# Optimization experiments

Measured on AMD Instinct MI355X. Metric: run time of the kernel, lower is better.

## Reference

```python
import jax, jax.numpy as jnp
import numpy as np

B, C, H, W = 16, 512, 32, 32
KC = C // 8  # key_channels = 64


def setup_inputs() -> dict:
    key = jax.random.key(0)
    ks = jax.random.split(key, 6)
    s_in = 1.0 / np.sqrt(C)
    return {
        "x": jax.random.normal(ks[0], (B, C, H, W), dtype=jnp.float32),
        "Wq": jax.random.normal(ks[1], (KC, C), dtype=jnp.float32) * s_in,
        "bq": jnp.zeros((KC,), dtype=jnp.float32),
        "Wk": jax.random.normal(ks[2], (KC, C), dtype=jnp.float32) * s_in,
        "bk": jnp.zeros((KC,), dtype=jnp.float32),
        "Wv": jax.random.normal(ks[3], (C, C), dtype=jnp.float32) * s_in,
        "bv": jnp.zeros((C,), dtype=jnp.float32),
        "Wo": jax.random.normal(ks[4], (C, C), dtype=jnp.float32) * s_in,
        "bo": jnp.zeros((C,), dtype=jnp.float32),
        "gamma": jnp.zeros((1,), dtype=jnp.float32),
    }


def reference(x, Wq, bq, Wk, bk, Wv, bv, Wo, bo, gamma):
    b, c, h, w = x.shape
    n = h * w
    kc = Wq.shape[0]
    xf = x.reshape(b, c, n)  # [B, C, N]
    # 1x1 convs == channel matmuls
    q = jnp.einsum('kc,bcn->bnk', Wq, xf) + bq  # [B, N, KC]
    k = jnp.einsum('kc,bcn->bkn', Wk, xf) + bk[None, :, None]  # [B, KC, N]
    v = jnp.einsum('vc,bcn->bnv', Wv, xf) + bv  # [B, N, C]
    scale = jnp.asarray(kc, x.dtype) ** -0.5
    att = jax.nn.softmax(jnp.einsum('bnk,bkm->bnm', q, k) * scale, axis=-1)  # [B, N, N]
    out = jnp.einsum('bnm,bmv->bnv', att, v)  # [B, N, C]
    out = jnp.einsum('cv,bnv->bcn', Wo, out) + bo[None, :, None]  # [B, C, N]
    out = gamma[0] * out + xf
    return out.reshape(b, c, h, w)
```

## Files before the change

### kernel.cpp

```cpp
#include <hip/hip_runtime.h>
#include <cstddef>


typedef unsigned short ushort_t;
typedef __attribute__((ext_vector_type(8))) short bf16x8;
typedef __attribute__((ext_vector_type(4))) float f32x4;

#define QSCALE 0.18033688011112042f

__device__ __forceinline__ ushort_t f2bf_t(float f) {
  return (ushort_t)(__float_as_uint(f) >> 16);
}
__device__ __forceinline__ unsigned pk2bf(float lo, float hi) {
  return __builtin_amdgcn_perm(__float_as_uint(hi), __float_as_uint(lo),
                               0x07060302u);
}

__device__ __forceinline__ void gload16(const ushort_t* g, ushort_t* l) {
  __builtin_amdgcn_global_load_lds(
      (const __attribute__((address_space(1))) void*)g,
      (__attribute__((address_space(3))) void*)l, 16, 0, 0);
}

template <int TM>
__device__ __forceinline__ void gemm_core(
    const ushort_t* __restrict__ A, int lda,
    const ushort_t* __restrict__ B, int ldb,
    int K, int m0, int n0,
    ushort_t* As, ushort_t* Bs, f32x4 (*acc)[4])
{
  constexpr int MT  = TM / 32;
  constexpr int WTM = TM / 2;
  const int t = threadIdx.x;
  const int lane = t & 63, quad = lane >> 4, l15 = lane & 15;
  const int w = t >> 6, wm = w >> 1, wn = w & 1;
  const int rr = (lane >> 3) & 7;
  const int gg = (lane & 7) ^ rr;

  #pragma unroll
  for (int i = 0; i < MT; ++i)
    #pragma unroll
    for (int j = 0; j < 4; ++j) acc[i][j] = (f32x4){0.f, 0.f, 0.f, 0.f};

  for (int k0 = 0; k0 < K; k0 += 64) {
    #pragma unroll
    for (int i = 0; i < TM / 32; ++i) {
      const int mrow = w * (TM / 4) + i * 8;
      gload16(A + (size_t)(m0 + mrow + rr) * lda + k0 + gg * 8, As + mrow * 64);
    }
    #pragma unroll
    for (int i = 0; i < 4; ++i) {
      const int mrow = w * 32 + i * 8;
      gload16(B + (size_t)(n0 + mrow + rr) * ldb + k0 + gg * 8, Bs + mrow * 64);
    }
    __syncthreads();
    #pragma unroll
    for (int kk = 0; kk < 2; ++kk) {
      const int gq = kk * 4 + quad;
      const int sg = (gq ^ (l15 & 7)) * 8;
      bf16x8 af[MT], bfr[4];
      #pragma unroll
      for (int i = 0; i < MT; ++i)
        af[i] = *(const bf16x8*)(As + (wm * WTM + i * 16 + l15) * 64 + sg);
      #pragma unroll
      for (int j = 0; j < 4; ++j)
        bfr[j] = *(const bf16x8*)(Bs + (wn * 64 + j * 16 + l15) * 64 + sg);
      #pragma unroll
      for (int i = 0; i < MT; ++i)
        #pragma unroll
        for (int j = 0; j < 4; ++j)
          acc[i][j] = __builtin_amdgcn_mfma_f32_16x16x32_bf16(
              af[i], bfr[j], acc[i][j], 0, 0, 0);
    }
    __syncthreads();
  }
}

template <int TM, class F>
__device__ __forceinline__ void store_bf16(
    ushort_t* lds, ushort_t* __restrict__ out, int ldo, int m0, int n0,
    f32x4 (*acc)[4], F f)
{
  constexpr int MT = TM / 32, WTM = TM / 2, SI = TM / 16;
  const int t = threadIdx.x;
  const int lane = t & 63, quad = lane >> 4, l15 = lane & 15;
  const int w = t >> 6, wm = w >> 1, wn = w & 1;
  #pragma unroll
  for (int i = 0; i < MT; ++i)
    #pragma unroll
    for (int j = 0; j < 4; ++j)
      #pragma unroll
      for (int r = 0; r < 4; ++r) {
        const int rl = wm * WTM + i * 16 + quad * 4 + r;
        const int cl = wn * 64 + j * 16 + l15;
        lds[rl * 136 + cl] = f2bf_t(f(i, j, r, rl, cl, acc[i][j][r]));
      }
  __syncthreads();
  #pragma unroll
  for (int i = 0; i < SI; ++i) {
    const int s = i * 256 + t, m = s >> 4, g = s & 15;
    const uint4 v = *(const uint4*)(lds + m * 136 + g * 8);
    *(uint4*)(out + (size_t)(m0 + m) * ldo + n0 + g * 8) = v;
  }
}

__global__ __launch_bounds__(256) void prep_x(
    const float* __restrict__ x,
    const float* __restrict__ Wq, const float* __restrict__ Wk,
    const float* __restrict__ Wv, const float* __restrict__ Wo,
    ushort_t* __restrict__ xbfT, ushort_t* __restrict__ Wqk,
    ushort_t* __restrict__ Wvb, ushort_t* __restrict__ Wob)
{
  __shared__ float T[64][65];
  const int t = threadIdx.x;
  if (blockIdx.y == 8) {
    const int id = blockIdx.z * 16 + blockIdx.x;
    #pragma unroll
    for (int p = 0; p < 5; ++p) {
      const int s = p * 256 + t;
      if (s < 1152) {
        const int u = id * 1152 + s;
        const int e = u * 2;
        float f0, f1;
        if (e < 32768)       { f0 = Wq[e];         f1 = Wq[e + 1]; }
        else if (e < 65536)  { f0 = Wk[e - 32768]; f1 = Wk[e - 32767]; }
        else if (e < 327680) { f0 = Wv[e - 65536]; f1 = Wv[e - 65535]; }
        else                 { f0 = Wo[e - 327680]; f1 = Wo[e - 327679]; }
        const unsigned pk = pk2bf(f0, f1);
        if (e < 65536)       *((unsigned*)Wqk + u) = pk;
        else if (e < 327680) *((unsigned*)Wvb + (u - 32768)) = pk;
        else                 *((unsigned*)Wob + (u - 163840)) = pk;
      }
    }
    return;
  }
  const int b = blockIdx.z, c0 = blockIdx.y * 64, n0 = blockIdx.x * 64;
  const float* xb = x + ((size_t)b * 512 + c0) * 1024 + n0;
  const int nj = t & 63, ci0 = t >> 6;
  #pragma unroll
  for (int p = 0; p < 16; ++p) {
    const int ci = p * 4 + ci0;
    T[ci][nj] = xb[(size_t)ci * 1024 + nj];
  }
  __syncthreads();
  const int c2 = (t & 31) * 2, nr0 = t >> 5;
  #pragma unroll
  for (int p = 0; p < 8; ++p) {
    const int nr = p * 8 + nr0;
    *(unsigned*)&xbfT[((size_t)b * 1024 + n0 + nr) * 512 + c0 + c2] =
        pk2bf(T[c2][nr], T[c2 + 1][nr]);
  }
}

__global__ __launch_bounds__(256) void k1_fused(
    const ushort_t* __restrict__ xbfT, const ushort_t* __restrict__ Wqk,
    const ushort_t* __restrict__ Wvb,
    const float* __restrict__ bq, const float* __restrict__ bk,
    const float* __restrict__ bv,
    ushort_t* __restrict__ qkt, ushort_t* __restrict__ vt2)
{
  __shared__ __align__(16) ushort_t lds[17408];
  const int bid = blockIdx.x;
  const int t = threadIdx.x, lane = t & 63, quad = lane >> 4, l15 = lane & 15;
  const int w = t >> 6, wm = w >> 1, wn = w & 1;
  if (bid < 512) {
    const int b = bid >> 5, my = (bid >> 3) & 3, nx = bid & 7;
    const int m0 = my * 128, n0 = nx * 128;
    f32x4 acc[4][4];
    gemm_core<128>(Wvb, 512, xbfT + (size_t)b * 524288, 512, 512, m0, n0,
                   lds, lds + 128 * 64, acc);
    float br[4][4];
    #pragma unroll
    for (int i = 0; i < 4; ++i)
      #pragma unroll
      for (int r = 0; r < 4; ++r)
        br[i][r] = bv[m0 + wm * 64 + i * 16 + quad * 4 + r];
    store_bf16<128>(lds, vt2 + (size_t)b * 524288, 1024, m0, n0, acc,
        [&](int i, int, int r, int, int, float v) { return v + br[i][r]; });
  } else {
    const int id = bid - 512, b = id >> 4, my = id & 15;
    const int m0 = my * 64;
    f32x4 acc[2][4];
    gemm_core<64>(xbfT + (size_t)b * 524288, 512, Wqk, 512, 512, m0, 0,
                  lds, lds + 64 * 64, acc);
    float bc[4], qs[4];
    #pragma unroll
    for (int j = 0; j < 4; ++j) {
      const int col = wn * 64 + j * 16 + l15;
      bc[j] = (col < 64) ? bq[col] : bk[col - 64];
      qs[j] = (col < 64) ? QSCALE : 1.0f;
    }
    store_bf16<64>(lds, qkt + (size_t)b * 131072, 128, m0, 0, acc,
        [&](int, int j, int, int, int, float v) { return (v + bc[j]) * qs[j]; });
  }
}

__global__ __launch_bounds__(256) void flash_attn(
    const ushort_t* __restrict__ qkt, const ushort_t* __restrict__ vt2,
    ushort_t* __restrict__ o1)
{
  __shared__ __align__(16) ushort_t buf[16896];
  __shared__ float lsum[64][2];
  ushort_t* Ks = buf;
  ushort_t* Vs = buf + 4096;
  ushort_t* Ps = buf + 12288;

  const int t = threadIdx.x;
  const int lane = t & 63, quad = lane >> 4, l15 = lane & 15;
  const int w = t >> 6, wm = w >> 1, wn = w & 1;
  const int rr = (lane >> 3) & 7, gg = (lane & 7) ^ rr;

  const unsigned lin = blockIdx.x;
  const unsigned wid = (lin & 7) * 128 + (lin >> 3);
  const int b  = wid >> 6;
  const int m0 = ((wid >> 2) & 15) * 64;
  const int c0 = (wid & 3) * 128;

  const ushort_t* qb = qkt + (size_t)b * 131072;
  const ushort_t* vb = vt2 + (size_t)b * 524288;

  #pragma unroll
  for (int i = 0; i < 2; ++i) {
    const int mrow = w * 16 + i * 8;
    gload16(qb + (size_t)(m0 + mrow + rr) * 128 + gg * 8, Ps + mrow * 64);
  }
  __syncthreads();
  bf16x8 af_q[2][2];
  #pragma unroll
  for (int kk = 0; kk < 2; ++kk) {
    const int sg = ((kk * 4 + quad) ^ (l15 & 7)) * 8;
    #pragma unroll
    for (int i = 0; i < 2; ++i)
      af_q[i][kk] = *(const bf16x8*)(Ps + (wm * 32 + i * 16 + l15) * 64 + sg);
  }

  f32x4 accO[2][4];
  #pragma unroll
  for (int i = 0; i < 2; ++i)
    #pragma unroll
    for (int j = 0; j < 4; ++j) accO[i][j] = (f32x4){0.f, 0.f, 0.f, 0.f};
  float rsum[2][4] = {{0.f, 0.f, 0.f, 0.f}, {0.f, 0.f, 0.f, 0.f}};

  ushort_t* ps_w = Ps + (wm * 32 + quad * 4) * 72 + wn * 32 + l15;

  #pragma unroll 1
  for (int mc = 0; mc < 1024; mc += 64) {
    __syncthreads();
    #pragma unroll
    for (int i = 0; i < 2; ++i) {
      const int mrow = w * 16 + i * 8;
      gload16(qb + (size_t)(mc + mrow + rr) * 128 + 64 + gg * 8, Ks + mrow * 64);
    }
    #pragma unroll
    for (int i = 0; i < 4; ++i) {
      const int mrow = w * 32 + i * 8;
      gload16(vb + (size_t)(c0 + mrow + rr) * 1024 + mc + gg * 8, Vs + mrow * 64);
    }
    __syncthreads();

    f32x4 accS[2][2];
    #pragma unroll
    for (int i = 0; i < 2; ++i)
      #pragma unroll
      for (int j = 0; j < 2; ++j) accS[i][j] = (f32x4){0.f, 0.f, 0.f, 0.f};
    #pragma unroll
    for (int kk = 0; kk < 2; ++kk) {
      const int sg = ((kk * 4 + quad) ^ (l15 & 7)) * 8;
      bf16x8 bk_[2];
      #pragma unroll
      for (int j = 0; j < 2; ++j)
        bk_[j] = *(const bf16x8*)(Ks + (wn * 32 + j * 16 + l15) * 64 + sg);
      #pragma unroll
      for (int i = 0; i < 2; ++i)
        #pragma unroll
        for (int j = 0; j < 2; ++j)
          accS[i][j] = __builtin_amdgcn_mfma_f32_16x16x32_bf16(
              af_q[i][kk], bk_[j], accS[i][j], 0, 0, 0);
    }
    #pragma unroll
    for (int i = 0; i < 2; ++i)
      #pragma unroll
      for (int j = 0; j < 2; ++j)
        #pragma unroll
        for (int r = 0; r < 4; ++r) {
          const float e = exp2f(accS[i][j][r]);
          rsum[i][r] += e;
          ps_w[(i * 16 + r) * 72 + j * 16] = f2bf_t(e);
        }
    __syncthreads();

    #pragma unroll
    for (int kk = 0; kk < 2; ++kk) {
      const int gq = kk * 4 + quad;
      const int sgv = (gq ^ (l15 & 7)) * 8;
      bf16x8 ap[2], bv_[4];
      #pragma unroll
      for (int i = 0; i < 2; ++i)
        ap[i] = *(const bf16x8*)(Ps + (wm * 32 + i * 16 + l15) * 72 + gq * 8);
      #pragma unroll
      for (int j = 0; j < 4; ++j)
        bv_[j] = *(const bf16x8*)(Vs + (wn * 64 + j * 16 + l15) * 64 + sgv);
      #pragma unroll
      for (int i = 0; i < 2; ++i)
        #pragma unroll
        for (int j = 0; j < 4; ++j)
          accO[i][j] = __builtin_amdgcn_mfma_f32_16x16x32_bf16(
              ap[i], bv_[j], accO[i][j], 0, 0, 0);
    }
  }

  #pragma unroll
  for (int i = 0; i < 2; ++i)
    #pragma unroll
    for (int r = 0; r < 4; ++r) {
      float s = rsum[i][r];
      #pragma unroll
      for (int d = 1; d < 16; d <<= 1) s += __shfl_xor(s, d, 16);
      if (l15 == 0) lsum[wm * 32 + i * 16 + quad * 4 + r][wn] = s;
    }
  __syncthreads();

  ushort_t* fl_b = buf;
  #pragma unroll
  for (int i = 0; i < 2; ++i)
    #pragma unroll
    for (int r = 0; r < 4; ++r) {
      const int row = wm * 32 + i * 16 + quad * 4 + r;
      const float inv = 1.0f / (lsum[row][0] + lsum[row][1]);
      #pragma unroll
      for (int j = 0; j < 4; ++j)
        fl_b[row * 136 + wn * 64 + j * 16 + l15] = f2bf_t(accO[i][j][r] * inv);
    }
  __syncthreads();
  #pragma unroll
  for (int p = 0; p < 4; ++p) {
    const int s = p * 256 + t, m = s >> 4, g = s & 15;
    const uint4 v = *(const uint4*)(fl_b + m * 136 + g * 8);
    *(uint4*)(o1 + ((size_t)b * 1024 + m0 + m) * 512 + c0 + g * 8) = v;
  }
}

__global__ __launch_bounds__(256) void k4_proj(
    const ushort_t* __restrict__ Wob, const ushort_t* __restrict__ o1,
    const float* __restrict__ bo, const float* __restrict__ gamma,
    const float* __restrict__ x, float* __restrict__ out)
{
  __shared__ __align__(16) ushort_t lds[128 * 136];
  const int b = blockIdx.z, m0 = blockIdx.y * 128, n0 = blockIdx.x * 128;
  f32x4 acc[4][4];
  gemm_core<128>(Wob, 512, o1 + (size_t)b * 524288, 512, 512, m0, n0,
                 lds, lds + 128 * 64, acc);
  const int t = threadIdx.x, lane = t & 63, quad = lane >> 4, l15 = lane & 15;
  const int w = t >> 6, wm = w >> 1, wn = w & 1;
  const float g = gamma[0];
  float br[4][4];
  #pragma unroll
  for (int i = 0; i < 4; ++i)
    #pragma unroll
    for (int r = 0; r < 4; ++r)
      br[i][r] = bo[m0 + wm * 64 + i * 16 + quad * 4 + r];
  float* fl = (float*)lds;
  #pragma unroll
  for (int h = 0; h < 2; ++h) {
    if (wm == h) {
      #pragma unroll
      for (int i = 0; i < 4; ++i)
        #pragma unroll
        for (int j = 0; j < 4; ++j)
          #pragma unroll
          for (int r = 0; r < 4; ++r)
            fl[(i * 16 + quad * 4 + r) * 132 + wn * 64 + j * 16 + l15] =
                g * (acc[i][j][r] + br[i][r]);
    }
    __syncthreads();
    #pragma unroll
    for (int i2 = 0; i2 < 8; ++i2) {
      const int s = i2 * 256 + t, m = s >> 5, c4 = s & 31;
      f32x4 v = *(const f32x4*)(fl + m * 132 + c4 * 4);
      const size_t gi = ((size_t)b * 512 + m0 + h * 64 + m) * 1024 + n0 + c4 * 4;
      const f32x4 xr = *(const f32x4*)(x + gi);
      v += xr;
      *(f32x4*)(out + gi) = v;
    }
    __syncthreads();
  }
}

extern "C" void kernel_launch(void* const* d_in, const int* in_sizes, int n_in,
                              void* d_out, int out_size, void* d_ws, size_t ws_size,
                              hipStream_t stream) {
  const float* x     = (const float*)d_in[0];
  const float* Wq    = (const float*)d_in[1];
  const float* bq    = (const float*)d_in[2];
  const float* Wk    = (const float*)d_in[3];
  const float* bk    = (const float*)d_in[4];
  const float* Wv    = (const float*)d_in[5];
  const float* bv    = (const float*)d_in[6];
  const float* Wo    = (const float*)d_in[7];
  const float* bo    = (const float*)d_in[8];
  const float* gamma = (const float*)d_in[9];
  float* out = (float*)d_out;

  char* wsp = (char*)d_ws;
  ushort_t* xbfT   = (ushort_t*)wsp;  wsp += (size_t)16 * 1024 * 512 * 2;
  ushort_t* Wqk_bf = (ushort_t*)wsp;  wsp += (size_t)128 * 512 * 2;
  ushort_t* Wv_bf  = (ushort_t*)wsp;  wsp += (size_t)512 * 512 * 2;
  ushort_t* Wo_bf  = (ushort_t*)wsp;  wsp += (size_t)512 * 512 * 2;
  ushort_t* qkt    = (ushort_t*)wsp;  wsp += (size_t)16 * 1024 * 128 * 2;
  ushort_t* vt2    = (ushort_t*)wsp;  wsp += (size_t)16 * 512 * 1024 * 2;
  ushort_t* o1     = xbfT;

  prep_x    <<<dim3(16, 9, 16), 256, 0, stream>>>(x, Wq, Wk, Wv, Wo,
                                                  xbfT, Wqk_bf, Wv_bf, Wo_bf);
  k1_fused  <<<768, 256, 0, stream>>>(xbfT, Wqk_bf, Wv_bf, bq, bk, bv, qkt, vt2);
  flash_attn<<<dim3(1024), 256, 0, stream>>>(qkt, vt2, o1);
  k4_proj   <<<dim3(8, 4, 16), 256, 0, stream>>>(Wo_bf, o1, bo, gamma, x, out);
}
```

Before: 195.6 us.

## Double-buffer K/V tiles in flash attention to overlap loads with compute

The flash attention loop now keeps two LDS buffers for the K, V and P tiles and issues the next tile's global-to-LDS loads before computing on the current one. The old per-iteration load-then-sync pattern is replaced by explicit waitcnt plus barrier pairs, cutting one barrier per iteration. It also swaps exp2f for the raw hardware exp2 builtin. LDS use roughly doubles, which may lower occupancy, and the manual waitcnt placement must stay correct.

```diff
diff --git a/kernel.cpp b/kernel.cpp
--- a/kernel.cpp
+++ b/kernel.cpp
@@ -199,11 +199,11 @@
     const ushort_t* __restrict__ qkt, const ushort_t* __restrict__ vt2,
     ushort_t* __restrict__ o1)
 {
-  __shared__ __align__(16) ushort_t buf[16896];
+  __shared__ __align__(16) ushort_t buf[33792];
   __shared__ float lsum[64][2];
-  ushort_t* Ks = buf;
-  ushort_t* Vs = buf + 4096;
-  ushort_t* Ps = buf + 12288;
+  ushort_t* Ks0 = buf;
+  ushort_t* Vs0 = buf + 8192;
+  ushort_t* Ps0 = buf + 24576;
 
   const int t = threadIdx.x;
   const int lane = t & 63, quad = lane >> 4, l15 = lane & 15;
@@ -222,17 +222,31 @@
   #pragma unroll
   for (int i = 0; i < 2; ++i) {
     const int mrow = w * 16 + i * 8;
-    gload16(qb + (size_t)(m0 + mrow + rr) * 128 + gg * 8, Ps + mrow * 64);
-  }
-  __syncthreads();
+    gload16(qb + (size_t)(m0 + mrow + rr) * 128 + gg * 8, Ps0 + mrow * 64);
+  }
+  asm volatile("s_waitcnt vmcnt(0)" ::: "memory");
+  __builtin_amdgcn_s_barrier();
+
   bf16x8 af_q[2][2];
   #pragma unroll
   for (int kk = 0; kk < 2; ++kk) {
     const int sg = ((kk * 4 + quad) ^ (l15 & 7)) * 8;
     #pragma unroll
     for (int i = 0; i < 2; ++i)
-      af_q[i][kk] = *(const bf16x8*)(Ps + (wm * 32 + i * 16 + l15) * 64 + sg);
-  }
+      af_q[i][kk] = *(const bf16x8*)(Ps0 + (wm * 32 + i * 16 + l15) * 64 + sg);
+  }
+
+  const ushort_t* kp = qb + (size_t)(w * 16 + rr) * 128 + 64 + gg * 8;
+  const ushort_t* vp = vb + (size_t)(c0 + w * 32 + rr) * 1024 + gg * 8;
+
+  #pragma unroll
+  for (int i = 0; i < 2; ++i)
+    gload16(kp + i * 1024, Ks0 + (w * 16 + i * 8) * 64);
+  #pragma unroll
+  for (int i = 0; i < 4; ++i)
+    gload16(vp + i * 8192, Vs0 + (w * 32 + i * 8) * 64);
+  asm volatile("s_waitcnt vmcnt(0) lgkmcnt(0)" ::: "memory");
+  __builtin_amdgcn_s_barrier();
 
   f32x4 accO[2][4];
   #pragma unroll
@@ -241,22 +255,30 @@
     for (int j = 0; j < 4; ++j) accO[i][j] = (f32x4){0.f, 0.f, 0.f, 0.f};
   float rsum[2][4] = {{0.f, 0.f, 0.f, 0.f}, {0.f, 0.f, 0.f, 0.f}};
 
-  ushort_t* ps_w = Ps + (wm * 32 + quad * 4) * 72 + wn * 32 + l15;
+  const int psw_off = (wm * 32 + quad * 4) * 72 + wn * 32 + l15;
+  const int sg0 = (quad ^ (l15 & 7)) * 8;
+  const int sg1 = ((4 + quad) ^ (l15 & 7)) * 8;
+
+  const ushort_t* kpn = kp + 8192;
+  const ushort_t* vpn = vp + 64;
+  int p = 0;
 
   #pragma unroll 1
   for (int mc = 0; mc < 1024; mc += 64) {
-    __syncthreads();
-    #pragma unroll
-    for (int i = 0; i < 2; ++i) {
-      const int mrow = w * 16 + i * 8;
-      gload16(qb + (size_t)(mc + mrow + rr) * 128 + 64 + gg * 8, Ks + mrow * 64);
-    }
-    #pragma unroll
-    for (int i = 0; i < 4; ++i) {
-      const int mrow = w * 32 + i * 8;
-      gload16(vb + (size_t)(c0 + mrow + rr) * 1024 + mc + gg * 8, Vs + mrow * 64);
-    }
-    __syncthreads();
+    ushort_t* Ksd = p ? Ks0 + 4096 : Ks0;
+    ushort_t* Vsd = p ? Vs0 + 8192 : Vs0;
+    ushort_t* Psd = p ? Ps0 + 4608 : Ps0;
+    ushort_t* Ksn = p ? Ks0 : Ks0 + 4096;
+    ushort_t* Vsn = p ? Vs0 : Vs0 + 8192;
+
+    if (mc < 960) {
+      #pragma unroll
+      for (int i = 0; i < 2; ++i)
+        gload16(kpn + i * 1024, Ksn + (w * 16 + i * 8) * 64);
+      #pragma unroll
+      for (int i = 0; i < 4; ++i)
+        gload16(vpn + i * 8192, Vsn + (w * 32 + i * 8) * 64);
+    }
 
     f32x4 accS[2][2];
     #pragma unroll
@@ -265,11 +287,11 @@
       for (int j = 0; j < 2; ++j) accS[i][j] = (f32x4){0.f, 0.f, 0.f, 0.f};
     #pragma unroll
     for (int kk = 0; kk < 2; ++kk) {
-      const int sg = ((kk * 4 + quad) ^ (l15 & 7)) * 8;
+      const int sg = kk ? sg1 : sg0;
       bf16x8 bk_[2];
       #pragma unroll
       for (int j = 0; j < 2; ++j)
-        bk_[j] = *(const bf16x8*)(Ks + (wn * 32 + j * 16 + l15) * 64 + sg);
+        bk_[j] = *(const bf16x8*)(Ksd + (wn * 32 + j * 16 + l15) * 64 + sg);
       #pragma unroll
       for (int i = 0; i < 2; ++i)
         #pragma unroll
@@ -277,29 +299,33 @@
           accS[i][j] = __builtin_amdgcn_mfma_f32_16x16x32_bf16(
               af_q[i][kk], bk_[j], accS[i][j], 0, 0, 0);
     }
+
+    ushort_t* psw = Psd + psw_off;
     #pragma unroll
     for (int i = 0; i < 2; ++i)
       #pragma unroll
       for (int j = 0; j < 2; ++j)
         #pragma unroll
         for (int r = 0; r < 4; ++r) {
-          const float e = exp2f(accS[i][j][r]);
+          const float e = __builtin_amdgcn_exp2f(accS[i][j][r]);
           rsum[i][r] += e;
-          ps_w[(i * 16 + r) * 72 + j * 16] = f2bf_t(e);
+          psw[(i * 16 + r) * 72 + j * 16] = f2bf_t(e);
         }
-    __syncthreads();
+
+    asm volatile("s_waitcnt lgkmcnt(0)" ::: "memory");
+    __builtin_amdgcn_s_barrier();
 
     #pragma unroll
     for (int kk = 0; kk < 2; ++kk) {
       const int gq = kk * 4 + quad;
-      const int sgv = (gq ^ (l15 & 7)) * 8;
+      const int sgv = kk ? sg1 : sg0;
       bf16x8 ap[2], bv_[4];
       #pragma unroll
       for (int i = 0; i < 2; ++i)
-        ap[i] = *(const bf16x8*)(Ps + (wm * 32 + i * 16 + l15) * 72 + gq * 8);
+        ap[i] = *(const bf16x8*)(Psd + (wm * 32 + i * 16 + l15) * 72 + gq * 8);
       #pragma unroll
       for (int j = 0; j < 4; ++j)
-        bv_[j] = *(const bf16x8*)(Vs + (wn * 64 + j * 16 + l15) * 64 + sgv);
+        bv_[j] = *(const bf16x8*)(Vsd + (wn * 64 + j * 16 + l15) * 64 + sgv);
       #pragma unroll
       for (int i = 0; i < 2; ++i)
         #pragma unroll
@@ -307,6 +333,13 @@
           accO[i][j] = __builtin_amdgcn_mfma_f32_16x16x32_bf16(
               ap[i], bv_[j], accO[i][j], 0, 0, 0);
     }
+
+    asm volatile("s_waitcnt vmcnt(0)" ::: "memory");
+    __builtin_amdgcn_s_barrier();
+
+    kpn += 8192;
+    vpn += 64;
+    p ^= 1;
   }
 
   #pragma unroll
@@ -333,8 +366,8 @@
     }
   __syncthreads();
   #pragma unroll
-  for (int p = 0; p < 4; ++p) {
-    const int s = p * 256 + t, m = s >> 4, g = s & 15;
+  for (int pp = 0; pp < 4; ++pp) {
+    const int s = pp * 256 + t, m = s >> 4, g = s & 15;
     const uint4 v = *(const uint4*)(fl_b + m * 136 + g * 8);
     *(uint4*)(o1 + ((size_t)b * 1024 + m0 + m) * 512 + c0 + g * 8) = v;
   }
```

Measured after the change: 188.9 us. 1.04x faster.
